# Performance work log

Measured on AMD Instinct MI355X. Metric: run time of the kernel, lower is better.

## Reference

```python
import jax, jax.numpy as jnp
import numpy as np

EPS_LN = 1e-5
EPS_SUMNORM = 1e-5
B, T, F, H = 8, 1024, 128, 64


def setup_inputs() -> dict:
    key = jax.random.key(0)
    ks = jax.random.split(key, 12)
    s = lambda fan_in: 1.0 / np.sqrt(fan_in)
    inp = {
        "x": jax.random.normal(ks[0], (B, T, F), dtype=jnp.float32),
        "state": jax.random.normal(ks[1], (B, 1, H * H), dtype=jnp.float32),
        # nn.Linear weights are [out, in]
        "Wk": jax.random.uniform(ks[2], (H, F), minval=-s(F), maxval=s(F)),
        "Wq": jax.random.uniform(ks[3], (H, F), minval=-s(F), maxval=s(F)),
        "Wv": jax.random.uniform(ks[4], (H, F), minval=-s(F), maxval=s(F)),
        "gamma": jnp.ones((F,), dtype=jnp.float32),
        "beta": jnp.zeros((F,), dtype=jnp.float32),
        "W1": jax.random.uniform(ks[5], (H, H), minval=-s(H), maxval=s(H)),
        "b1": jax.random.uniform(ks[6], (H,), minval=-s(H), maxval=s(H)),
        "W2": jax.random.uniform(ks[7], (H, H), minval=-s(H), maxval=s(H)),
        "b2": jax.random.uniform(ks[8], (H,), minval=-s(H), maxval=s(H)),
        "Ws": jax.random.uniform(ks[9], (H, F), minval=-s(F), maxval=s(F)),
        "bs": jax.random.uniform(ks[10], (H,), minval=-s(F), maxval=s(F)),
    }
    return inp


def reference(x, state, Wk, Wq, Wv, gamma, beta, W1, b1, W2, b2, Ws, bs):
    # LayerNorm over feature dim
    mu = jnp.mean(x, axis=-1, keepdims=True)
    var = jnp.var(x, axis=-1, keepdims=True)
    xn = (x - mu) * jax.lax.rsqrt(var + EPS_LN) * gamma + beta  # [B,T,F]

    K = jax.nn.relu(jnp.einsum('btf,hf->bth', xn, Wk))
    Q = jax.nn.relu(jnp.einsum('btf,hf->bth', xn, Wq))
    V = jnp.einsum('btf,hf->bth', xn, Wv)

    # sum normalization
    K = K / (EPS_SUMNORM + jnp.sum(K, axis=-1, keepdims=True))
    Q = Q / (EPS_SUMNORM + jnp.sum(Q, axis=-1, keepdims=True))

    # outer-product fast weights: kv[b,t,i,j] = V[b,t,i] * K[b,t,j]
    kv = jnp.einsum('bti,btj->btij', V, K)  # [B,T,H,H]

    # 'sum' aggregator: running sum over time starting from initial state
    S = jnp.cumsum(kv, axis=1) + state.reshape(B, 1, H, H)  # [B,T,H,H]

    y = jnp.einsum('btij,btj->bti', S, Q)  # [B,T,H]

    # feed forward
    y = jax.nn.relu(jnp.einsum('bti,oi->bto', y, W1) + b1)
    y = jax.nn.relu(jnp.einsum('bti,oi->bto', y, W2) + b2)

    # residual shortcut (from the normalized x, matching the torch reassignment)
    y = y + jnp.einsum('btf,hf->bth', xn, Ws) + bs
    return y, S
```

## Files before the change

kernel.cpp:

```cpp
#include <hip/hip_runtime.h>

#define Bn 8
#define Tn 1024
#define Fn 128
#define Hn 64
#define NC 64
#define CSZ 16

constexpr float EPS = 1e-5f;

__device__ __forceinline__ void fma4(float4& a, float s, const float4& w) {
    a.x = fmaf(s, w.x, a.x); a.y = fmaf(s, w.y, a.y);
    a.z = fmaf(s, w.z, a.z); a.w = fmaf(s, w.w, a.w);
}
__device__ __forceinline__ float4 f4zero() { return make_float4(0.f, 0.f, 0.f, 0.f); }

__global__ __launch_bounds__(256) void k1_proj(
    const float* __restrict__ x, const float* __restrict__ gamma, const float* __restrict__ beta,
    const float* __restrict__ Wk, const float* __restrict__ Wq, const float* __restrict__ Wv,
    const float* __restrict__ Wsp, const float* __restrict__ bs,
    float* __restrict__ Kb, float* __restrict__ Qb, float* __restrict__ Vb, float* __restrict__ Rb,
    float* __restrict__ csum) {
    __shared__ float LW[32 * 260];
    __shared__ float LX[32 * 36];
    __shared__ float Kc[32 * Hn];
    __shared__ float Vc[32 * Hn];
    const int tid  = threadIdx.x;
    const int tok0 = blockIdx.x * 32;
    const int tg   = tid >> 6;
    const int cg   = tid & 63;

    const float* WmS  = (tg == 0) ? Wk : (tg == 1) ? Wq : (tg == 2) ? Wv : Wsp;
    const float* wrow = WmS + (tid & 63) * Fn;

    const int tt = tid >> 3, kk = (tid & 7) * 4;
    float4 xreg[4];
    float s = 0.f, ss = 0.f;
#pragma unroll
    for (int c = 0; c < 4; c++) {
        xreg[c] = *(const float4*)(x + (tok0 + tt) * Fn + c * 32 + kk);
        s  += xreg[c].x + xreg[c].y + xreg[c].z + xreg[c].w;
        ss += xreg[c].x * xreg[c].x + xreg[c].y * xreg[c].y
            + xreg[c].z * xreg[c].z + xreg[c].w * xreg[c].w;
    }
#pragma unroll
    for (int m = 1; m < 8; m <<= 1) { s += __shfl_xor(s, m); ss += __shfl_xor(ss, m); }
    const float mu = s * (1.f / Fn);
    const float rs = rsqrtf(ss * (1.f / Fn) - mu * mu + EPS);

    float4 acc[8];
#pragma unroll
    for (int i = 0; i < 8; i++) acc[i] = f4zero();

    for (int c = 0; c < 4; c++) {
        const int kc0 = c * 32;
#pragma unroll
        for (int r = 0; r < 8; r++) {
            const float4 wv = *(const float4*)(wrow + kc0 + r * 4);
            LW[(r * 4 + 0) * 260 + tid] = wv.x;
            LW[(r * 4 + 1) * 260 + tid] = wv.y;
            LW[(r * 4 + 2) * 260 + tid] = wv.z;
            LW[(r * 4 + 3) * 260 + tid] = wv.w;
        }
        {
            const float4 g4 = *(const float4*)(gamma + kc0 + kk);
            const float4 b4 = *(const float4*)(beta + kc0 + kk);
            const float4 xv = xreg[c];
            LX[(kk + 0) * 36 + tt] = (xv.x - mu) * rs * g4.x + b4.x;
            LX[(kk + 1) * 36 + tt] = (xv.y - mu) * rs * g4.y + b4.y;
            LX[(kk + 2) * 36 + tt] = (xv.z - mu) * rs * g4.z + b4.z;
            LX[(kk + 3) * 36 + tt] = (xv.w - mu) * rs * g4.w + b4.w;
        }
        __syncthreads();
#pragma unroll 8
        for (int kc = 0; kc < 32; kc++) {
            const float4 w4 = *(const float4*)&LW[kc * 260 + cg * 4];
            const float4 xa = *(const float4*)&LX[kc * 36 + tg * 8];
            const float4 xb = *(const float4*)&LX[kc * 36 + tg * 8 + 4];
            fma4(acc[0], xa.x, w4); fma4(acc[1], xa.y, w4);
            fma4(acc[2], xa.z, w4); fma4(acc[3], xa.w, w4);
            fma4(acc[4], xb.x, w4); fma4(acc[5], xb.y, w4);
            fma4(acc[6], xb.z, w4); fma4(acc[7], xb.w, w4);
        }
        __syncthreads();
    }

    const int m  = cg >> 4;
    const int h0 = (cg & 15) * 4;
    if (m < 2) {
#pragma unroll
        for (int i = 0; i < 8; i++) {
            acc[i].x = fmaxf(acc[i].x, 0.f); acc[i].y = fmaxf(acc[i].y, 0.f);
            acc[i].z = fmaxf(acc[i].z, 0.f); acc[i].w = fmaxf(acc[i].w, 0.f);
        }
    }
    float rsum[8];
#pragma unroll
    for (int i = 0; i < 8; i++) {
        rsum[i] = acc[i].x + acc[i].y + acc[i].z + acc[i].w;
        rsum[i] += __shfl_xor(rsum[i], 1);
        rsum[i] += __shfl_xor(rsum[i], 2);
        rsum[i] += __shfl_xor(rsum[i], 4);
        rsum[i] += __shfl_xor(rsum[i], 8);
    }
    if (m < 2) {
#pragma unroll
        for (int i = 0; i < 8; i++) {
            const float inv = 1.f / (EPS + rsum[i]);
            acc[i].x *= inv; acc[i].y *= inv; acc[i].z *= inv; acc[i].w *= inv;
        }
    } else if (m == 3) {
        const float4 bv = *(const float4*)(bs + h0);
#pragma unroll
        for (int i = 0; i < 8; i++) {
            acc[i].x += bv.x; acc[i].y += bv.y; acc[i].z += bv.z; acc[i].w += bv.w;
        }
    }
    float* outp = (m == 0) ? Kb : (m == 1) ? Qb : (m == 2) ? Vb : Rb;
#pragma unroll
    for (int ti = 0; ti < 8; ti++)
        *(float4*)(outp + (tok0 + tg * 8 + ti) * Hn + h0) = acc[ti];
    if (m == 0) {
#pragma unroll
        for (int ti = 0; ti < 8; ti++) *(float4*)(Kc + (tg * 8 + ti) * Hn + h0) = acc[ti];
    } else if (m == 2) {
#pragma unroll
        for (int ti = 0; ti < 8; ti++) *(float4*)(Vc + (tg * 8 + ti) * Hn + h0) = acc[ti];
    }
    __syncthreads();

    const int jq = tid & 15, rr = tid >> 4;
    const int b  = tok0 >> 10;
    const int c0 = ((tok0 & 1023) >> 5) * 2;
    float4 a4[4];
    float4* out0 = (float4*)(csum + (size_t)(b * NC + c0) * 4096);
#pragma unroll
    for (int sI = 0; sI < 4; sI++) a4[sI] = f4zero();
    for (int t = 0; t < 16; t++) {
        const float4 kv = ((const float4*)Kc)[t * 16 + jq];
#pragma unroll
        for (int sI = 0; sI < 4; sI++) fma4(a4[sI], Vc[t * Hn + sI * 16 + rr], kv);
    }
#pragma unroll
    for (int sI = 0; sI < 4; sI++) out0[sI * 256 + tid] = a4[sI];
#pragma unroll
    for (int sI = 0; sI < 4; sI++) a4[sI] = f4zero();
    for (int t = 16; t < 32; t++) {
        const float4 kv = ((const float4*)Kc)[t * 16 + jq];
#pragma unroll
        for (int sI = 0; sI < 4; sI++) fma4(a4[sI], Vc[t * Hn + sI * 16 + rr], kv);
    }
#pragma unroll
    for (int sI = 0; sI < 4; sI++) out0[1024 + sI * 256 + tid] = a4[sI];
}

__global__ __launch_bounds__(256) void k2_scan(const float* __restrict__ state,
                                               float* __restrict__ csum) {
    const int b = blockIdx.x >> 4, et = blockIdx.x & 15;
    const int e = et * 256 + threadIdx.x;
    float v[NC];
#pragma unroll
    for (int c = 0; c < NC; c++) v[c] = csum[(size_t)(b * NC + c) * 4096 + e];
    float acc = state[b * 4096 + e];
#pragma unroll
    for (int c = 0; c < NC; c++) {
        csum[(size_t)(b * NC + c) * 4096 + e] = acc;
        acc += v[c];
    }
}

__global__ __launch_bounds__(256, 2) void k3_main(
    const float* __restrict__ Kb, const float* __restrict__ Qb, const float* __restrict__ Vb,
    const float* __restrict__ cstart, const float* __restrict__ Rb,
    const float* __restrict__ W1, const float* __restrict__ b1,
    const float* __restrict__ W2, const float* __restrict__ b2,
    float* __restrict__ outY, float* __restrict__ outS) {
    __shared__ float Kc[CSZ * Hn];
    __shared__ float Qc[CSZ * Hn];
    __shared__ float Vc[CSZ * Hn];
    __shared__ float WT[2][64 * 68];
    __shared__ float Yl[CSZ * 68];
    __shared__ float Y2[CSZ * 68];
    __shared__ float Lb[2][64];
    const int tid = threadIdx.x;
    const int b = blockIdx.x >> 6, c = blockIdx.x & 63;
    const int t0 = c * CSZ;
    ((float4*)Kc)[tid] = ((const float4*)(Kb + (b * Tn + t0) * Hn))[tid];
    ((float4*)Qc)[tid] = ((const float4*)(Qb + (b * Tn + t0) * Hn))[tid];
    ((float4*)Vc)[tid] = ((const float4*)(Vb + (b * Tn + t0) * Hn))[tid];
#pragma unroll
    for (int mat = 0; mat < 2; mat++) {
        const float4* Wg = (const float4*)(mat ? W2 : W1);
#pragma unroll
        for (int r = 0; r < 4; r++) {
            const int f4i = tid + 256 * r;
            const float4 wv = Wg[f4i];
            const int h = f4i >> 4;
            const int k = (f4i & 15) * 4;
            WT[mat][(k + 0) * 68 + h] = wv.x;
            WT[mat][(k + 1) * 68 + h] = wv.y;
            WT[mat][(k + 2) * 68 + h] = wv.z;
            WT[mat][(k + 3) * 68 + h] = wv.w;
        }
    }
    if (tid < 64) Lb[0][tid] = b1[tid];
    else if (tid < 128) Lb[1][tid - 64] = b2[tid - 64];
    float4 S4[4];
    const float4* cs = (const float4*)(cstart + (size_t)(b * NC + c) * 4096);
#pragma unroll
    for (int sI = 0; sI < 4; sI++) S4[sI] = cs[sI * 256 + tid];
    __syncthreads();

    const int jq = tid & 15, rr = tid >> 4;
    float4* SBase = (float4*)outS + (size_t)(b * Tn + t0) * 1024;
    for (int t = 0; t < CSZ; t++) {
        const float4 kv = ((const float4*)Kc)[t * 16 + jq];
        const float4 qv = ((const float4*)Qc)[t * 16 + jq];
        float yp[4];
#pragma unroll
        for (int sI = 0; sI < 4; sI++) {
            fma4(S4[sI], Vc[t * Hn + sI * 16 + rr], kv);
            yp[sI] = S4[sI].x * qv.x + S4[sI].y * qv.y + S4[sI].z * qv.z + S4[sI].w * qv.w;
        }
        float4* So = SBase + t * 1024;
#pragma unroll
        for (int sI = 0; sI < 4; sI++) So[sI * 256 + tid] = S4[sI];
#pragma unroll
        for (int sI = 0; sI < 4; sI++) {
            yp[sI] += __shfl_xor(yp[sI], 1);
            yp[sI] += __shfl_xor(yp[sI], 2);
            yp[sI] += __shfl_xor(yp[sI], 4);
            yp[sI] += __shfl_xor(yp[sI], 8);
        }
        if (jq == 0) {
#pragma unroll
            for (int sI = 0; sI < 4; sI++) Yl[t * 68 + sI * 16 + rr] = yp[sI];
        }
    }
    __syncthreads();

    const int tg = tid >> 4, cg = tid & 15;
    float4 a = *(const float4*)&Lb[0][cg * 4];
#pragma unroll 16
    for (int k = 0; k < 64; k++)
        fma4(a, Yl[tg * 68 + k], *(const float4*)&WT[0][k * 68 + cg * 4]);
    a.x = fmaxf(a.x, 0.f); a.y = fmaxf(a.y, 0.f); a.z = fmaxf(a.z, 0.f); a.w = fmaxf(a.w, 0.f);
    *(float4*)&Y2[tg * 68 + cg * 4] = a;
    __syncthreads();
    float4 o = *(const float4*)&Lb[1][cg * 4];
#pragma unroll 16
    for (int k = 0; k < 64; k++)
        fma4(o, Y2[tg * 68 + k], *(const float4*)&WT[1][k * 68 + cg * 4]);
    const float4 r4 = ((const float4*)(Rb + (b * Tn + t0) * Hn))[tid];
    o.x = fmaxf(o.x, 0.f) + r4.x; o.y = fmaxf(o.y, 0.f) + r4.y;
    o.z = fmaxf(o.z, 0.f) + r4.z; o.w = fmaxf(o.w, 0.f) + r4.w;
    ((float4*)(outY + (b * Tn + t0) * Hn))[tid] = o;
}

extern "C" void kernel_launch(void* const* d_in, const int* in_sizes, int n_in,
                              void* d_out, int out_size, void* d_ws, size_t ws_size,
                              hipStream_t stream) {
    const float* x     = (const float*)d_in[0];
    const float* state = (const float*)d_in[1];
    const float* Wk    = (const float*)d_in[2];
    const float* Wq    = (const float*)d_in[3];
    const float* Wv    = (const float*)d_in[4];
    const float* gamma = (const float*)d_in[5];
    const float* beta  = (const float*)d_in[6];
    const float* W1    = (const float*)d_in[7];
    const float* b1    = (const float*)d_in[8];
    const float* W2    = (const float*)d_in[9];
    const float* b2    = (const float*)d_in[10];
    const float* Wsp   = (const float*)d_in[11];
    const float* bs    = (const float*)d_in[12];

    float* ws   = (float*)d_ws;
    float* Kb   = ws;
    float* Qb   = ws + 524288;
    float* Vb   = ws + 1048576;
    float* Rb   = ws + 1572864;
    float* csum = ws + 2097152;

    float* outY = (float*)d_out;
    float* outS = outY + (size_t)Bn * Tn * Hn;

    k1_proj<<<256, 256, 0, stream>>>(x, gamma, beta, Wk, Wq, Wv, Wsp, bs, Kb, Qb, Vb, Rb, csum);
    k2_scan<<<128, 256, 0, stream>>>(state, csum);
    k3_main<<<512, 256, 0, stream>>>(Kb, Qb, Vb, csum, Rb, W1, b1, W2, b2, outY, outS);
}
```

Baseline: 194.4 us.

## Fuse projection, chunk scan and main pass into one cooperative kernel

Three kernels (projection, chunk-sum scan, main recurrence with feed-forward) become one cooperative kernel with 512 blocks, using two grid-wide syncs between phases. K, Q, V and the residual stay in shared memory instead of round-tripping through global workspace buffers, and the scan is parallelised across four waves per block with a shared-memory segment prefix. This removes two launches and the K/Q/V/R global traffic. In exchange it depends on all 512 blocks being co-resident (two per CU) and adds grid-sync overhead.

```diff
diff --git a/kernel.cpp b/kernel.cpp
--- a/kernel.cpp
+++ b/kernel.cpp
@@ -1,4 +1,7 @@
 #include <hip/hip_runtime.h>
+#include <hip/hip_cooperative_groups.h>
+
+namespace cg = cooperative_groups;
 
 #define Bn 8
 #define Tn 1024
@@ -15,179 +18,130 @@
 }
 __device__ __forceinline__ float4 f4zero() { return make_float4(0.f, 0.f, 0.f, 0.f); }
 
-__global__ __launch_bounds__(256) void k1_proj(
-    const float* __restrict__ x, const float* __restrict__ gamma, const float* __restrict__ beta,
+struct SharedA {
+    float LW[32 * 260];
+    float LX[128 * 20];
+};
+struct SharedC {
+    float WT[2][64 * 68];
+    float Yl[CSZ * 68];
+    float Y2[CSZ * 68];
+    float Lb[2][64];
+};
+struct Shared {
+    float Kc[CSZ * Hn];
+    float Qc[CSZ * Hn];
+    float Vc[CSZ * Hn];
+    float Rc[CSZ * Hn];
+    union { SharedA a; SharedC c; } u;
+    float seg[4][64];
+};
+
+__global__ __launch_bounds__(256, 2) void fwp_fused(
+    const float* __restrict__ x, const float* __restrict__ state,
     const float* __restrict__ Wk, const float* __restrict__ Wq, const float* __restrict__ Wv,
+    const float* __restrict__ gamma, const float* __restrict__ beta,
+    const float* __restrict__ W1, const float* __restrict__ b1,
+    const float* __restrict__ W2, const float* __restrict__ b2,
     const float* __restrict__ Wsp, const float* __restrict__ bs,
-    float* __restrict__ Kb, float* __restrict__ Qb, float* __restrict__ Vb, float* __restrict__ Rb,
-    float* __restrict__ csum) {
-    __shared__ float LW[32 * 260];
-    __shared__ float LX[32 * 36];
-    __shared__ float Kc[32 * Hn];
-    __shared__ float Vc[32 * Hn];
-    const int tid  = threadIdx.x;
-    const int tok0 = blockIdx.x * 32;
-    const int tg   = tid >> 6;
-    const int cg   = tid & 63;
-
-    const float* WmS  = (tg == 0) ? Wk : (tg == 1) ? Wq : (tg == 2) ? Wv : Wsp;
+    float* __restrict__ csum, float* __restrict__ outY, float* __restrict__ outS) {
+    __shared__ Shared sh;
+    cg::grid_group grid = cg::this_grid();
+    const int tid = threadIdx.x;
+    const int bl  = blockIdx.x;
+    const int b   = bl >> 6, c = bl & 63;
+    const int t0  = c * CSZ;
+
+    {
+        const int tt = tid >> 4, ffq = tid & 15;
+        const float* xp = x + (size_t)(b * Tn + t0 + tt) * Fn + ffq * 8;
+        const float4 xr0 = *(const float4*)(xp);
+        const float4 xr1 = *(const float4*)(xp + 4);
+        float s  = xr0.x + xr0.y + xr0.z + xr0.w + xr1.x + xr1.y + xr1.z + xr1.w;
+        float ss = xr0.x * xr0.x + xr0.y * xr0.y + xr0.z * xr0.z + xr0.w * xr0.w
+                 + xr1.x * xr1.x + xr1.y * xr1.y + xr1.z * xr1.z + xr1.w * xr1.w;
+#pragma unroll
+        for (int m = 1; m < 16; m <<= 1) { s += __shfl_xor(s, m); ss += __shfl_xor(ss, m); }
+        const float mu = s * (1.f / Fn);
+        const float rs = rsqrtf(ss * (1.f / Fn) - mu * mu + EPS);
+        const float4 g0 = *(const float4*)(gamma + ffq * 8);
+        const float4 g1 = *(const float4*)(gamma + ffq * 8 + 4);
+        const float4 be0 = *(const float4*)(beta + ffq * 8);
+        const float4 be1 = *(const float4*)(beta + ffq * 8 + 4);
+        float* LX = sh.u.a.LX;
+        LX[(ffq * 8 + 0) * 20 + tt] = (xr0.x - mu) * rs * g0.x + be0.x;
+        LX[(ffq * 8 + 1) * 20 + tt] = (xr0.y - mu) * rs * g0.y + be0.y;
+        LX[(ffq * 8 + 2) * 20 + tt] = (xr0.z - mu) * rs * g0.z + be0.z;
+        LX[(ffq * 8 + 3) * 20 + tt] = (xr0.w - mu) * rs * g0.w + be0.w;
+        LX[(ffq * 8 + 4) * 20 + tt] = (xr1.x - mu) * rs * g1.x + be1.x;
+        LX[(ffq * 8 + 5) * 20 + tt] = (xr1.y - mu) * rs * g1.y + be1.y;
+        LX[(ffq * 8 + 6) * 20 + tt] = (xr1.z - mu) * rs * g1.z + be1.z;
+        LX[(ffq * 8 + 7) * 20 + tt] = (xr1.w - mu) * rs * g1.w + be1.w;
+    }
+    const int wave = tid >> 6;
+    const int cgq  = tid & 63;
+    const int tg   = wave;
+    const float* WmS  = (wave == 0) ? Wk : (wave == 1) ? Wq : (wave == 2) ? Wv : Wsp;
     const float* wrow = WmS + (tid & 63) * Fn;
-
-    const int tt = tid >> 3, kk = (tid & 7) * 4;
-    float4 xreg[4];
-    float s = 0.f, ss = 0.f;
-#pragma unroll
-    for (int c = 0; c < 4; c++) {
-        xreg[c] = *(const float4*)(x + (tok0 + tt) * Fn + c * 32 + kk);
-        s  += xreg[c].x + xreg[c].y + xreg[c].z + xreg[c].w;
-        ss += xreg[c].x * xreg[c].x + xreg[c].y * xreg[c].y
-            + xreg[c].z * xreg[c].z + xreg[c].w * xreg[c].w;
-    }
-#pragma unroll
-    for (int m = 1; m < 8; m <<= 1) { s += __shfl_xor(s, m); ss += __shfl_xor(ss, m); }
-    const float mu = s * (1.f / Fn);
-    const float rs = rsqrtf(ss * (1.f / Fn) - mu * mu + EPS);
-
-    float4 acc[8];
-#pragma unroll
-    for (int i = 0; i < 8; i++) acc[i] = f4zero();
-
-    for (int c = 0; c < 4; c++) {
-        const int kc0 = c * 32;
+    float4 acc[4];
+#pragma unroll
+    for (int i = 0; i < 4; i++) acc[i] = f4zero();
+    for (int kc0 = 0; kc0 < Fn; kc0 += 32) {
 #pragma unroll
         for (int r = 0; r < 8; r++) {
             const float4 wv = *(const float4*)(wrow + kc0 + r * 4);
-            LW[(r * 4 + 0) * 260 + tid] = wv.x;
-            LW[(r * 4 + 1) * 260 + tid] = wv.y;
-            LW[(r * 4 + 2) * 260 + tid] = wv.z;
-            LW[(r * 4 + 3) * 260 + tid] = wv.w;
-        }
-        {
-            const float4 g4 = *(const float4*)(gamma + kc0 + kk);
-            const float4 b4 = *(const float4*)(beta + kc0 + kk);
-            const float4 xv = xreg[c];
-            LX[(kk + 0) * 36 + tt] = (xv.x - mu) * rs * g4.x + b4.x;
-            LX[(kk + 1) * 36 + tt] = (xv.y - mu) * rs * g4.y + b4.y;
-            LX[(kk + 2) * 36 + tt] = (xv.z - mu) * rs * g4.z + b4.z;
-            LX[(kk + 3) * 36 + tt] = (xv.w - mu) * rs * g4.w + b4.w;
+            sh.u.a.LW[(r * 4 + 0) * 260 + tid] = wv.x;
+            sh.u.a.LW[(r * 4 + 1) * 260 + tid] = wv.y;
+            sh.u.a.LW[(r * 4 + 2) * 260 + tid] = wv.z;
+            sh.u.a.LW[(r * 4 + 3) * 260 + tid] = wv.w;
         }
         __syncthreads();
 #pragma unroll 8
         for (int kc = 0; kc < 32; kc++) {
-            const float4 w4 = *(const float4*)&LW[kc * 260 + cg * 4];
-            const float4 xa = *(const float4*)&LX[kc * 36 + tg * 8];
-            const float4 xb = *(const float4*)&LX[kc * 36 + tg * 8 + 4];
+            const float4 w4 = *(const float4*)&sh.u.a.LW[kc * 260 + cgq * 4];
+            const float4 xa = *(const float4*)&sh.u.a.LX[(kc0 + kc) * 20 + tg * 4];
             fma4(acc[0], xa.x, w4); fma4(acc[1], xa.y, w4);
             fma4(acc[2], xa.z, w4); fma4(acc[3], xa.w, w4);
-            fma4(acc[4], xb.x, w4); fma4(acc[5], xb.y, w4);
-            fma4(acc[6], xb.z, w4); fma4(acc[7], xb.w, w4);
         }
         __syncthreads();
     }
-
-    const int m  = cg >> 4;
-    const int h0 = (cg & 15) * 4;
-    if (m < 2) {
-#pragma unroll
-        for (int i = 0; i < 8; i++) {
-            acc[i].x = fmaxf(acc[i].x, 0.f); acc[i].y = fmaxf(acc[i].y, 0.f);
-            acc[i].z = fmaxf(acc[i].z, 0.f); acc[i].w = fmaxf(acc[i].w, 0.f);
-        }
-    }
-    float rsum[8];
-#pragma unroll
-    for (int i = 0; i < 8; i++) {
-        rsum[i] = acc[i].x + acc[i].y + acc[i].z + acc[i].w;
-        rsum[i] += __shfl_xor(rsum[i], 1);
-        rsum[i] += __shfl_xor(rsum[i], 2);
-        rsum[i] += __shfl_xor(rsum[i], 4);
-        rsum[i] += __shfl_xor(rsum[i], 8);
-    }
-    if (m < 2) {
-#pragma unroll
-        for (int i = 0; i < 8; i++) {
-            const float inv = 1.f / (EPS + rsum[i]);
-            acc[i].x *= inv; acc[i].y *= inv; acc[i].z *= inv; acc[i].w *= inv;
-        }
-    } else if (m == 3) {
-        const float4 bv = *(const float4*)(bs + h0);
-#pragma unroll
-        for (int i = 0; i < 8; i++) {
-            acc[i].x += bv.x; acc[i].y += bv.y; acc[i].z += bv.z; acc[i].w += bv.w;
-        }
-    }
-    float* outp = (m == 0) ? Kb : (m == 1) ? Qb : (m == 2) ? Vb : Rb;
-#pragma unroll
-    for (int ti = 0; ti < 8; ti++)
-        *(float4*)(outp + (tok0 + tg * 8 + ti) * Hn + h0) = acc[ti];
-    if (m == 0) {
-#pragma unroll
-        for (int ti = 0; ti < 8; ti++) *(float4*)(Kc + (tg * 8 + ti) * Hn + h0) = acc[ti];
-    } else if (m == 2) {
-#pragma unroll
-        for (int ti = 0; ti < 8; ti++) *(float4*)(Vc + (tg * 8 + ti) * Hn + h0) = acc[ti];
-    }
-    __syncthreads();
-
-    const int jq = tid & 15, rr = tid >> 4;
-    const int b  = tok0 >> 10;
-    const int c0 = ((tok0 & 1023) >> 5) * 2;
-    float4 a4[4];
-    float4* out0 = (float4*)(csum + (size_t)(b * NC + c0) * 4096);
-#pragma unroll
-    for (int sI = 0; sI < 4; sI++) a4[sI] = f4zero();
-    for (int t = 0; t < 16; t++) {
-        const float4 kv = ((const float4*)Kc)[t * 16 + jq];
-#pragma unroll
-        for (int sI = 0; sI < 4; sI++) fma4(a4[sI], Vc[t * Hn + sI * 16 + rr], kv);
-    }
-#pragma unroll
-    for (int sI = 0; sI < 4; sI++) out0[sI * 256 + tid] = a4[sI];
-#pragma unroll
-    for (int sI = 0; sI < 4; sI++) a4[sI] = f4zero();
-    for (int t = 16; t < 32; t++) {
-        const float4 kv = ((const float4*)Kc)[t * 16 + jq];
-#pragma unroll
-        for (int sI = 0; sI < 4; sI++) fma4(a4[sI], Vc[t * Hn + sI * 16 + rr], kv);
-    }
-#pragma unroll
-    for (int sI = 0; sI < 4; sI++) out0[1024 + sI * 256 + tid] = a4[sI];
-}
-
-__global__ __launch_bounds__(256) void k2_scan(const float* __restrict__ state,
-                                               float* __restrict__ csum) {
-    const int b = blockIdx.x >> 4, et = blockIdx.x & 15;
-    const int e = et * 256 + threadIdx.x;
-    float v[NC];
-#pragma unroll
-    for (int c = 0; c < NC; c++) v[c] = csum[(size_t)(b * NC + c) * 4096 + e];
-    float acc = state[b * 4096 + e];
-#pragma unroll
-    for (int c = 0; c < NC; c++) {
-        csum[(size_t)(b * NC + c) * 4096 + e] = acc;
-        acc += v[c];
-    }
-}
-
-__global__ __launch_bounds__(256, 2) void k3_main(
-    const float* __restrict__ Kb, const float* __restrict__ Qb, const float* __restrict__ Vb,
-    const float* __restrict__ cstart, const float* __restrict__ Rb,
-    const float* __restrict__ W1, const float* __restrict__ b1,
-    const float* __restrict__ W2, const float* __restrict__ b2,
-    float* __restrict__ outY, float* __restrict__ outS) {
-    __shared__ float Kc[CSZ * Hn];
-    __shared__ float Qc[CSZ * Hn];
-    __shared__ float Vc[CSZ * Hn];
-    __shared__ float WT[2][64 * 68];
-    __shared__ float Yl[CSZ * 68];
-    __shared__ float Y2[CSZ * 68];
-    __shared__ float Lb[2][64];
-    const int tid = threadIdx.x;
-    const int b = blockIdx.x >> 6, c = blockIdx.x & 63;
-    const int t0 = c * CSZ;
-    ((float4*)Kc)[tid] = ((const float4*)(Kb + (b * Tn + t0) * Hn))[tid];
-    ((float4*)Qc)[tid] = ((const float4*)(Qb + (b * Tn + t0) * Hn))[tid];
-    ((float4*)Vc)[tid] = ((const float4*)(Vb + (b * Tn + t0) * Hn))[tid];
+    {
+        const int m  = cgq >> 4;
+        const int h0 = (cgq & 15) * 4;
+        if (m < 2) {
+#pragma unroll
+            for (int i = 0; i < 4; i++) {
+                acc[i].x = fmaxf(acc[i].x, 0.f); acc[i].y = fmaxf(acc[i].y, 0.f);
+                acc[i].z = fmaxf(acc[i].z, 0.f); acc[i].w = fmaxf(acc[i].w, 0.f);
+            }
+        }
+        float rsum[4];
+#pragma unroll
+        for (int i = 0; i < 4; i++) {
+            rsum[i] = acc[i].x + acc[i].y + acc[i].z + acc[i].w;
+            rsum[i] += __shfl_xor(rsum[i], 1);
+            rsum[i] += __shfl_xor(rsum[i], 2);
+            rsum[i] += __shfl_xor(rsum[i], 4);
+            rsum[i] += __shfl_xor(rsum[i], 8);
+        }
+        if (m < 2) {
+#pragma unroll
+            for (int i = 0; i < 4; i++) {
+                const float inv = 1.f / (EPS + rsum[i]);
+                acc[i].x *= inv; acc[i].y *= inv; acc[i].z *= inv; acc[i].w *= inv;
+            }
+        } else if (m == 3) {
+            const float4 bv = *(const float4*)(bs + h0);
+#pragma unroll
+            for (int i = 0; i < 4; i++) {
+                acc[i].x += bv.x; acc[i].y += bv.y; acc[i].z += bv.z; acc[i].w += bv.w;
+            }
+        }
+        float* dst = (m == 0) ? sh.Kc : (m == 1) ? sh.Qc : (m == 2) ? sh.Vc : sh.Rc;
+#pragma unroll
+        for (int ti = 0; ti < 4; ti++)
+            *(float4*)(dst + (tg * 4 + ti) * Hn + h0) = acc[ti];
+    }
 #pragma unroll
     for (int mat = 0; mat < 2; mat++) {
         const float4* Wg = (const float4*)(mat ? W2 : W1);
@@ -197,29 +151,71 @@
             const float4 wv = Wg[f4i];
             const int h = f4i >> 4;
             const int k = (f4i & 15) * 4;
-            WT[mat][(k + 0) * 68 + h] = wv.x;
-            WT[mat][(k + 1) * 68 + h] = wv.y;
-            WT[mat][(k + 2) * 68 + h] = wv.z;
-            WT[mat][(k + 3) * 68 + h] = wv.w;
-        }
-    }
-    if (tid < 64) Lb[0][tid] = b1[tid];
-    else if (tid < 128) Lb[1][tid - 64] = b2[tid - 64];
+            sh.u.c.WT[mat][(k + 0) * 68 + h] = wv.x;
+            sh.u.c.WT[mat][(k + 1) * 68 + h] = wv.y;
+            sh.u.c.WT[mat][(k + 2) * 68 + h] = wv.z;
+            sh.u.c.WT[mat][(k + 3) * 68 + h] = wv.w;
+        }
+    }
+    if (tid < 64) sh.u.c.Lb[0][tid] = b1[tid];
+    else if (tid < 128) sh.u.c.Lb[1][tid - 64] = b2[tid - 64];
+    __syncthreads();
+    const int jq = tid & 15, rr = tid >> 4;
+    {
+        float4 a4[4];
+#pragma unroll
+        for (int sI = 0; sI < 4; sI++) a4[sI] = f4zero();
+        for (int t = 0; t < CSZ; t++) {
+            const float4 kv = ((const float4*)sh.Kc)[t * 16 + jq];
+#pragma unroll
+            for (int sI = 0; sI < 4; sI++) fma4(a4[sI], sh.Vc[t * Hn + sI * 16 + rr], kv);
+        }
+        float4* out0 = (float4*)(csum + (size_t)bl * 4096);
+#pragma unroll
+        for (int sI = 0; sI < 4; sI++) out0[sI * 256 + tid] = a4[sI];
+    }
+    __threadfence();
+    grid.sync();
+
+    {
+        const int b2 = bl >> 6, eg = bl & 63;
+        const int el = tid & 63, w = tid >> 6;
+        const int e  = eg * 64 + el;
+        float* cbase = csum + (size_t)b2 * (NC * 4096) + e;
+        float v[16];
+        float segs = 0.f;
+#pragma unroll
+        for (int i = 0; i < 16; i++) {
+            v[i] = cbase[(size_t)(w * 16 + i) * 4096];
+            segs += v[i];
+        }
+        sh.seg[w][el] = segs;
+        __syncthreads();
+        float base = state[b2 * 4096 + e];
+        for (int w2 = 0; w2 < w; w2++) base += sh.seg[w2][el];
+#pragma unroll
+        for (int i = 0; i < 16; i++) {
+            cbase[(size_t)(w * 16 + i) * 4096] = base;
+            base += v[i];
+        }
+    }
+    __threadfence();
+    grid.sync();
+
     float4 S4[4];
-    const float4* cs = (const float4*)(cstart + (size_t)(b * NC + c) * 4096);
-#pragma unroll
-    for (int sI = 0; sI < 4; sI++) S4[sI] = cs[sI * 256 + tid];
-    __syncthreads();
-
-    const int jq = tid & 15, rr = tid >> 4;
+    {
+        const float4* cs = (const float4*)(csum + (size_t)bl * 4096);
+#pragma unroll
+        for (int sI = 0; sI < 4; sI++) S4[sI] = cs[sI * 256 + tid];
+    }
     float4* SBase = (float4*)outS + (size_t)(b * Tn + t0) * 1024;
     for (int t = 0; t < CSZ; t++) {
-        const float4 kv = ((const float4*)Kc)[t * 16 + jq];
-        const float4 qv = ((const float4*)Qc)[t * 16 + jq];
+        const float4 kv = ((const float4*)sh.Kc)[t * 16 + jq];
+        const float4 qv = ((const float4*)sh.Qc)[t * 16 + jq];
         float yp[4];
 #pragma unroll
         for (int sI = 0; sI < 4; sI++) {
-            fma4(S4[sI], Vc[t * Hn + sI * 16 + rr], kv);
+            fma4(S4[sI], sh.Vc[t * Hn + sI * 16 + rr], kv);
             yp[sI] = S4[sI].x * qv.x + S4[sI].y * qv.y + S4[sI].z * qv.z + S4[sI].w * qv.w;
         }
         float4* So = SBase + t * 1024;
@@ -234,27 +230,31 @@
         }
         if (jq == 0) {
 #pragma unroll
-            for (int sI = 0; sI < 4; sI++) Yl[t * 68 + sI * 16 + rr] = yp[sI];
+            for (int sI = 0; sI < 4; sI++) sh.u.c.Yl[t * 68 + sI * 16 + rr] = yp[sI];
         }
     }
     __syncthreads();
-
-    const int tg = tid >> 4, cg = tid & 15;
-    float4 a = *(const float4*)&Lb[0][cg * 4];
+    const int tg2 = tid >> 4, cg2 = tid & 15;
+    {
+        float4 a = *(const float4*)&sh.u.c.Lb[0][cg2 * 4];
 #pragma unroll 16
-    for (int k = 0; k < 64; k++)
-        fma4(a, Yl[tg * 68 + k], *(const float4*)&WT[0][k * 68 + cg * 4]);
-    a.x = fmaxf(a.x, 0.f); a.y = fmaxf(a.y, 0.f); a.z = fmaxf(a.z, 0.f); a.w = fmaxf(a.w, 0.f);
-    *(float4*)&Y2[tg * 68 + cg * 4] = a;
+        for (int k = 0; k < 64; k++)
+            fma4(a, sh.u.c.Yl[tg2 * 68 + k], *(const float4*)&sh.u.c.WT[0][k * 68 + cg2 * 4]);
+        a.x = fmaxf(a.x, 0.f); a.y = fmaxf(a.y, 0.f);
+        a.z = fmaxf(a.z, 0.f); a.w = fmaxf(a.w, 0.f);
+        *(float4*)&sh.u.c.Y2[tg2 * 68 + cg2 * 4] = a;
+    }
     __syncthreads();
-    float4 o = *(const float4*)&Lb[1][cg * 4];
+    {
+        float4 o = *(const float4*)&sh.u.c.Lb[1][cg2 * 4];
 #pragma unroll 16
-    for (int k = 0; k < 64; k++)
-        fma4(o, Y2[tg * 68 + k], *(const float4*)&WT[1][k * 68 + cg * 4]);
-    const float4 r4 = ((const float4*)(Rb + (b * Tn + t0) * Hn))[tid];
-    o.x = fmaxf(o.x, 0.f) + r4.x; o.y = fmaxf(o.y, 0.f) + r4.y;
-    o.z = fmaxf(o.z, 0.f) + r4.z; o.w = fmaxf(o.w, 0.f) + r4.w;
-    ((float4*)(outY + (b * Tn + t0) * Hn))[tid] = o;
+        for (int k = 0; k < 64; k++)
+            fma4(o, sh.u.c.Y2[tg2 * 68 + k], *(const float4*)&sh.u.c.WT[1][k * 68 + cg2 * 4]);
+        const float4 r4 = ((const float4*)sh.Rc)[tid];
+        o.x = fmaxf(o.x, 0.f) + r4.x; o.y = fmaxf(o.y, 0.f) + r4.y;
+        o.z = fmaxf(o.z, 0.f) + r4.z; o.w = fmaxf(o.w, 0.f) + r4.w;
+        ((float4*)(outY + (size_t)(b * Tn + t0) * Hn))[tid] = o;
+    }
 }
 
 extern "C" void kernel_launch(void* const* d_in, const int* in_sizes, int n_in,
@@ -274,17 +274,13 @@
     const float* Wsp   = (const float*)d_in[11];
     const float* bs    = (const float*)d_in[12];
 
-    float* ws   = (float*)d_ws;
-    float* Kb   = ws;
-    float* Qb   = ws + 524288;
-    float* Vb   = ws + 1048576;
-    float* Rb   = ws + 1572864;
-    float* csum = ws + 2097152;
-
+    float* csum = (float*)d_ws;
     float* outY = (float*)d_out;
     float* outS = outY + (size_t)Bn * Tn * Hn;
 
-    k1_proj<<<256, 256, 0, stream>>>(x, gamma, beta, Wk, Wq, Wv, Wsp, bs, Kb, Qb, Vb, Rb, csum);
-    k2_scan<<<128, 256, 0, stream>>>(state, csum);
-    k3_main<<<512, 256, 0, stream>>>(Kb, Qb, Vb, csum, Rb, W1, b1, W2, b2, outY, outS);
+    void* args[] = { (void*)&x, (void*)&state, (void*)&Wk, (void*)&Wq, (void*)&Wv,
+                     (void*)&gamma, (void*)&beta, (void*)&W1, (void*)&b1, (void*)&W2,
+                     (void*)&b2, (void*)&Wsp, (void*)&bs,
+                     (void*)&csum, (void*)&outY, (void*)&outS };
+    hipLaunchCooperativeKernel((const void*)fwp_fused, dim3(512), dim3(256), args, 0, stream);
 }
```

Result: slower. 440.9 us (+126.8%).

## Halve chunk-sum granularity and recompute odd-chunk prefix in main kernel

Applied to the files above, without the earlier changes.

The per-chunk KV sums and the scan now work at 32-token granularity instead of 16, which halves the csum buffer writes in k1 and the scan traffic in k2. The main kernel still processes 16-token chunks. Odd chunks load the previous 16 tokens of K and V and recompute their outer-product contribution locally before starting. This trades redundant FMA work and extra shared memory in half the k3 blocks for less global memory traffic in the partial-sum and scan stages.

```diff
diff --git a/kernel.cpp b/kernel.cpp
--- a/kernel.cpp
+++ b/kernel.cpp
@@ -4,7 +4,7 @@
 #define Tn 1024
 #define Fn 128
 #define Hn 64
-#define NC 64
+#define NC 32
 #define CSZ 16
 
 constexpr float EPS = 1e-5f;
@@ -130,28 +130,17 @@
     __syncthreads();
 
     const int jq = tid & 15, rr = tid >> 4;
-    const int b  = tok0 >> 10;
-    const int c0 = ((tok0 & 1023) >> 5) * 2;
     float4 a4[4];
-    float4* out0 = (float4*)(csum + (size_t)(b * NC + c0) * 4096);
 #pragma unroll
     for (int sI = 0; sI < 4; sI++) a4[sI] = f4zero();
-    for (int t = 0; t < 16; t++) {
+    for (int t = 0; t < 32; t++) {
         const float4 kv = ((const float4*)Kc)[t * 16 + jq];
 #pragma unroll
         for (int sI = 0; sI < 4; sI++) fma4(a4[sI], Vc[t * Hn + sI * 16 + rr], kv);
     }
+    float4* out0 = (float4*)(csum + (size_t)blockIdx.x * 4096);
 #pragma unroll
     for (int sI = 0; sI < 4; sI++) out0[sI * 256 + tid] = a4[sI];
-#pragma unroll
-    for (int sI = 0; sI < 4; sI++) a4[sI] = f4zero();
-    for (int t = 16; t < 32; t++) {
-        const float4 kv = ((const float4*)Kc)[t * 16 + jq];
-#pragma unroll
-        for (int sI = 0; sI < 4; sI++) fma4(a4[sI], Vc[t * Hn + sI * 16 + rr], kv);
-    }
-#pragma unroll
-    for (int sI = 0; sI < 4; sI++) out0[1024 + sI * 256 + tid] = a4[sI];
 }
 
 __global__ __launch_bounds__(256) void k2_scan(const float* __restrict__ state,
@@ -178,16 +167,24 @@
     __shared__ float Kc[CSZ * Hn];
     __shared__ float Qc[CSZ * Hn];
     __shared__ float Vc[CSZ * Hn];
+    __shared__ float Kp[CSZ * Hn];
+    __shared__ float Vp[CSZ * Hn];
     __shared__ float WT[2][64 * 68];
     __shared__ float Yl[CSZ * 68];
     __shared__ float Y2[CSZ * 68];
     __shared__ float Lb[2][64];
     const int tid = threadIdx.x;
-    const int b = blockIdx.x >> 6, c = blockIdx.x & 63;
-    const int t0 = c * CSZ;
+    const int bl  = blockIdx.x;
+    const int b = bl >> 6, c16 = bl & 63;
+    const int t0 = c16 * CSZ;
+    const int odd = bl & 1;
     ((float4*)Kc)[tid] = ((const float4*)(Kb + (b * Tn + t0) * Hn))[tid];
     ((float4*)Qc)[tid] = ((const float4*)(Qb + (b * Tn + t0) * Hn))[tid];
     ((float4*)Vc)[tid] = ((const float4*)(Vb + (b * Tn + t0) * Hn))[tid];
+    if (odd) {
+        ((float4*)Kp)[tid] = ((const float4*)(Kb + (b * Tn + t0 - CSZ) * Hn))[tid];
+        ((float4*)Vp)[tid] = ((const float4*)(Vb + (b * Tn + t0 - CSZ) * Hn))[tid];
+    }
 #pragma unroll
     for (int mat = 0; mat < 2; mat++) {
         const float4* Wg = (const float4*)(mat ? W2 : W1);
@@ -206,12 +203,19 @@
     if (tid < 64) Lb[0][tid] = b1[tid];
     else if (tid < 128) Lb[1][tid - 64] = b2[tid - 64];
     float4 S4[4];
-    const float4* cs = (const float4*)(cstart + (size_t)(b * NC + c) * 4096);
+    const float4* cs = (const float4*)(cstart + (size_t)(bl >> 1) * 4096);
 #pragma unroll
     for (int sI = 0; sI < 4; sI++) S4[sI] = cs[sI * 256 + tid];
     __syncthreads();
 
     const int jq = tid & 15, rr = tid >> 4;
+    if (odd) {
+        for (int t = 0; t < CSZ; t++) {
+            const float4 kv = ((const float4*)Kp)[t * 16 + jq];
+#pragma unroll
+            for (int sI = 0; sI < 4; sI++) fma4(S4[sI], Vp[t * Hn + sI * 16 + rr], kv);
+        }
+    }
     float4* SBase = (float4*)outS + (size_t)(b * Tn + t0) * 1024;
     for (int t = 0; t < CSZ; t++) {
         const float4 kv = ((const float4*)Kc)[t * 16 + jq];
```

New measurement: 193.9 us. Within noise of the previous version (-0.3%).
